# Performance work log

Measured on AMD Instinct MI355X. Metric: run time of the kernel, lower is better.

The kernel has to match this reference:

```python
import jax, jax.numpy as jnp
import numpy as np

EPS = 1e-5  # float32 path of the torch LayerNorm variants


def setup_inputs() -> dict:
    key = jax.random.key(0)
    ks = jax.random.split(key, 12)
    b, c, t, h, w = 2, 512, 16, 32, 32
    heads, dim_head = 8, 64
    inner = heads * dim_head            # 512
    cpb = c // 2                        # 256 (ContinuousPositionBias hidden dim)
    inner_ff = int(c * 4 * 2 / 3)       # 1365 (GEGLU FeedForward)
    s = 0.02
    return {
        "x": jax.random.normal(ks[0], (b, c, t, h, w), jnp.float32),
        "framerate": 4,
        "g_norm": jnp.ones((c,), jnp.float32),
        "Wq": jax.random.normal(ks[1], (c, inner), jnp.float32) * s,
        "Wkv": jax.random.normal(ks[2], (c, 2 * inner), jnp.float32) * s,
        "Wo": jax.random.normal(ks[3], (inner, c), jnp.float32) * s,
        "pos_emb": jax.random.normal(ks[4], (1, 30, c), jnp.float32),
        "fr_emb": jax.random.normal(ks[5], (1, 30, c), jnp.float32),
        "cpb_w1": jax.random.normal(ks[6], (1, cpb), jnp.float32) * s,
        "cpb_b1": jnp.zeros((cpb,), jnp.float32),
        "cpb_w2": jax.random.normal(ks[7], (cpb, cpb), jnp.float32) * s,
        "cpb_b2": jnp.zeros((cpb,), jnp.float32),
        "cpb_w3": jax.random.normal(ks[8], (cpb, 8), jnp.float32) * s,
        "cpb_b3": jnp.zeros((8,), jnp.float32),
        "Win": jax.random.normal(ks[9], (c, 2 * inner_ff), jnp.float32) * s,
        "chan_g": jnp.ones((inner_ff,), jnp.float32),
        "Wout": jax.random.normal(ks[10], (inner_ff, c), jnp.float32) * s,
    }


def _forward(x, framerate, g_norm, Wq, Wkv, Wo, pos_emb, fr_emb,
             cpb_w1, cpb_b1, cpb_w2, cpb_b2, cpb_w3, cpb_b3,
             Win, chan_g, Wout):
    b, c, t, hh, ww = x.shape
    heads = cpb_b3.shape[0]
    dim_head = Wq.shape[1] // heads
    scale = dim_head ** -0.5

    # ---- ContinuousPositionBias over time (num_dims=1, log_dist) ----
    pos = jnp.arange(t)
    rel = (pos[:, None] - pos[None, :])[..., None].astype(x.dtype)   # [t, t, 1]
    rel = jnp.sign(rel) * jnp.log(jnp.abs(rel) + 1.0)
    hb = jax.nn.silu(rel @ cpb_w1 + cpb_b1)
    hb = jax.nn.silu(hb @ cpb_w2 + cpb_b2)
    bias = jnp.transpose(hb @ cpb_w3 + cpb_b3, (2, 0, 1))            # [H, t, t]

    # ---- temporal attention: fold spatial dims into batch ----
    xt = jnp.transpose(x, (0, 3, 4, 2, 1)).reshape(b * hh * ww, t, c)  # [B, t, c]
    xe = xt + pos_emb[:, :t] + fr_emb[:, framerate - 1:framerate]
    # LayerNorm as written in the source: stats over dim=1 (the token axis)
    mean = jnp.mean(xe, axis=1, keepdims=True)
    var = jnp.var(xe, axis=1, keepdims=True)
    xn = (xe - mean) * jax.lax.rsqrt(jnp.maximum(var, EPS)) * g_norm

    q = (xn @ Wq).reshape(-1, t, heads, dim_head).transpose(0, 2, 1, 3)  # [B,H,t,d]
    k, v = jnp.split(xn @ Wkv, 2, axis=-1)
    k = k.reshape(-1, t, heads, dim_head).transpose(0, 2, 1, 3)
    v = v.reshape(-1, t, heads, dim_head).transpose(0, 2, 1, 3)

    sim = jnp.einsum('bhid,bhjd->bhij', q * scale, k) + bias[None]
    attn = jax.nn.softmax(sim, axis=-1)
    o = jnp.einsum('bhij,bhjd->bhid', attn, v)
    o = o.transpose(0, 2, 1, 3).reshape(-1, t, heads * dim_head) @ Wo
    xt = o + xt  # residual
    x = jnp.transpose(xt.reshape(b, hh, ww, t, c), (0, 4, 3, 1, 2))  # [b,c,t,h,w]

    # ---- GEGLU FeedForward (1x1x1 convs) with token shift over time ----
    y = jnp.einsum('bcthw,co->bothw', x, Win)
    y1, gate = jnp.split(y, 2, axis=1)
    y = y1 * jax.nn.gelu(gate, approximate=False)
    half = (y.shape[1] + 1) // 2  # torch.chunk: first chunk gets ceil
    ya, yb = y[:, :half], y[:, half:]
    yb = jnp.pad(yb, ((0, 0), (0, 0), (1, 0), (0, 0), (0, 0)))[:, :, :-1]
    y = jnp.concatenate([ya, yb], axis=1)
    m = jnp.mean(y, axis=1, keepdims=True)
    vv = jnp.var(y, axis=1, keepdims=True)
    y = (y - m) * jax.lax.rsqrt(jnp.maximum(vv, EPS)) * chan_g[None, :, None, None, None]
    y = jnp.einsum('bcthw,co->bothw', y, Wout)
    return y + x


def reference(x, framerate, g_norm, Wq, Wkv, Wo, pos_emb, fr_emb,
              cpb_w1, cpb_b1, cpb_w2, cpb_b2, cpb_w3, cpb_b3,
              Win, chan_g, Wout):
    return _forward(x, framerate, g_norm, Wq, Wkv, Wo, pos_emb, fr_emb,
                    cpb_w1, cpb_b1, cpb_w2, cpb_b2, cpb_w3, cpb_b3,
                    Win, chan_g, Wout)
```

## Files before the change

kernel.cpp:

```cpp
#include <hip/hip_runtime.h>

using u16 = unsigned short;
using f32x4 = __attribute__((ext_vector_type(4))) float;
using short8 = __attribute__((ext_vector_type(8))) short;

__device__ __forceinline__ float bf2f(u16 u) {
    union { unsigned int i; float f; } v; v.i = ((unsigned int)u) << 16; return v.f;
}
__device__ __forceinline__ u16 f2bf(float f) {
    union { float f; unsigned int i; } v; v.f = f;
    unsigned int u = v.i;
    u += 0x7fffu + ((u >> 16) & 1u);
    return (u16)(u >> 16);
}
__device__ __forceinline__ void gload16(const u16* g, u16* l) {
    __builtin_amdgcn_global_load_lds((const __attribute__((address_space(1))) void*)g,
                                     (__attribute__((address_space(3))) void*)l, 16, 0, 0);
}

__global__ __launch_bounds__(256) void prologue_all(
    const float* __restrict__ x, const int* __restrict__ frp,
    const float* __restrict__ g_norm, const float* __restrict__ pos_emb,
    const float* __restrict__ fr_emb,
    const float* __restrict__ Wq, const float* __restrict__ Wkv,
    const float* __restrict__ Wo, const float* __restrict__ Win,
    const float* __restrict__ Wout, const float* __restrict__ cg,
    const float* __restrict__ w1, const float* __restrict__ b1,
    const float* __restrict__ w2, const float* __restrict__ b2,
    const float* __restrict__ w3, const float* __restrict__ b3,
    u16* __restrict__ xn, u16* __restrict__ xt,
    u16* __restrict__ wqkvt, u16* __restrict__ wot,
    u16* __restrict__ winp, u16* __restrict__ woutt,
    float* __restrict__ ssum, float* __restrict__ bias)
{
    __shared__ __align__(16) char smem[256 * 36 * 2];
    const int bid = blockIdx.x;
    const int tid = threadIdx.x;
    if (bid < 2048) {
        u16* tile = (u16*)smem;
        const int b = bid >> 10, rem = bid & 1023;
        const int hw0 = (rem >> 4) << 4;
        const int c0 = (rem & 15) << 5;
        const int hwl = tid & 15, cl = tid >> 4;
        const int fr = frp[0] - 1;
        float v[2][16], mean2[2], ri2[2], gg2[2], fv2[2];
        for (int cp = 0; cp < 2; ++cp) {
            const int c = c0 + cl + (cp << 4);
            const float* xp = x + (size_t)(b * 512 + c) * 16384 + hw0 + hwl;
            const float fv = fr_emb[fr * 512 + c];
            float s1 = 0.f, s2 = 0.f;
#pragma unroll
            for (int t = 0; t < 16; ++t) {
                float xv = xp[t * 1024];
                v[cp][t] = xv;
                float xe = xv + pos_emb[t * 512 + c] + fv;
                s1 += xe; s2 += xe * xe;
            }
            float m = s1 * 0.0625f;
            float var = s2 * 0.0625f - m * m;
            mean2[cp] = m; ri2[cp] = rsqrtf(fmaxf(var, 1e-5f));
            gg2[cp] = g_norm[c]; fv2[cp] = fv;
        }
        for (int cp = 0; cp < 2; ++cp) {
            const int c = c0 + cl + (cp << 4);
#pragma unroll
            for (int t = 0; t < 16; ++t) {
                float xe = v[cp][t] + pos_emb[t * 512 + c] + fv2[cp];
                tile[((t << 4) + hwl) * 36 + cl + (cp << 4)] = f2bf((xe - mean2[cp]) * ri2[cp] * gg2[cp]);
            }
        }
        __syncthreads();
        for (int it = 0; it < 8; ++it) {
            int idx = it * 256 + tid;
            int rowl = idx >> 3, c4 = (idx & 7) << 2;
            size_t p = (size_t)b * 16384 + (size_t)(rowl >> 4) * 1024 + hw0 + (rowl & 15);
            uint2 d = *(const uint2*)(tile + rowl * 36 + c4);
            *(uint2*)(xn + p * 512 + c0 + c4) = d;
        }
        __syncthreads();
        for (int cp = 0; cp < 2; ++cp)
#pragma unroll
            for (int t = 0; t < 16; ++t)
                tile[((t << 4) + hwl) * 36 + cl + (cp << 4)] = f2bf(v[cp][t]);
        __syncthreads();
        for (int it = 0; it < 8; ++it) {
            int idx = it * 256 + tid;
            int rowl = idx >> 3, c4 = (idx & 7) << 2;
            size_t p = (size_t)b * 16384 + (size_t)(rowl >> 4) * 1024 + hw0 + (rowl & 15);
            uint2 d = *(const uint2*)(tile + rowl * 36 + c4);
            *(uint2*)(xt + p * 512 + c0 + c4) = d;
        }
        return;
    }
    if (bid < 2832) {
        float* tf = (float*)smem;
        const u16* dummy = nullptr; (void)dummy;
        int r0, c0, ldout;
        u16* dst;
        int kind;
        int tt;
        if (bid < 2240)      { tt = bid - 2048; r0 = (tt >> 3) << 6; c0 = (tt & 7) << 6;  dst = wqkvt; ldout = 512;  kind = 0; }
        else if (bid < 2304) { tt = bid - 2240; r0 = (tt >> 3) << 6; c0 = (tt & 7) << 6;  dst = wot;   ldout = 512;  kind = 1; }
        else if (bid < 2656) { tt = bid - 2304; r0 = (tt >> 3) << 6; c0 = (tt & 7) << 6;  dst = winp;  ldout = 512;  kind = 2; }
        else                 { tt = bid - 2656; r0 = (tt / 22) << 6; c0 = (tt % 22) << 6; dst = woutt; ldout = 1408; kind = 3; }
#pragma unroll 1
        for (int i = 0; i < 16; ++i) {
            int idx = tid + (i << 8);
            int cl = idx >> 6, rl = idx & 63;
            int r = r0 + rl, c = c0 + cl;
            float v;
            if (kind == 0) {
                v = (r < 512) ? Wq[c * 512 + r] : Wkv[c * 1024 + (r - 512)];
            } else if (kind == 1) {
                v = Wo[c * 512 + r];
            } else if (kind == 2) {
                int jj = ((r >> 5) << 4) + (r & 15);
                int gate = (r >> 4) & 1;
                v = (jj < 1365) ? Win[c * 2730 + jj + gate * 1365] : 0.f;
            } else {
                v = (c < 1365) ? Wout[c * 512 + r] * cg[c] : 0.f;
            }
            tf[rl * 65 + cl] = v;
        }
        __syncthreads();
        for (int i = 0; i < 4; ++i) {
            int idx = tid + (i << 8);
            int rl = idx >> 4, c4 = (idx & 15) << 2;
            const float* tp = tf + rl * 65 + c4;
            unsigned int lo = ((unsigned int)f2bf(tp[1]) << 16) | f2bf(tp[0]);
            unsigned int hi = ((unsigned int)f2bf(tp[3]) << 16) | f2bf(tp[2]);
            *(uint2*)(dst + (size_t)(r0 + rl) * ldout + c0 + c4) = make_uint2(lo, hi);
        }
        return;
    }
    if (bid < 2960) {
        int c = ((bid - 2832) << 2) + (tid >> 6);
        int lane = tid & 63;
        float s = 0.f;
        for (int j = lane; j < 1365; j += 64) s += Wout[j * 512 + c] * cg[j];
        for (int off = 32; off; off >>= 1) s += __shfl_xor(s, off);
        if (lane == 0) ssum[c] = s;
        return;
    }
    {
        float* h1 = (float*)smem;
        float* h2 = h1 + 256;
        int rc = bid - 2960;
        int ti = rc >> 4, tj = rc & 15;
        int j = tid;
        float r = (float)(ti - tj);
        float rl = (r > 0.f) ? logf(r + 1.f) : ((r < 0.f) ? -logf(1.f - r) : 0.f);
        float a = rl * w1[j] + b1[j];
        h1[j] = a / (1.f + __expf(-a));
        __syncthreads();
        float acc = b2[j];
        for (int k = 0; k < 256; ++k) acc += h1[k] * w2[k * 256 + j];
        h2[j] = acc / (1.f + __expf(-acc));
        __syncthreads();
        if (j < 8) {
            float ab = b3[j];
            for (int k = 0; k < 256; ++k) ab += h2[k] * w3[k * 8 + j];
            bias[j * 256 + ti * 16 + tj] = ab;
        }
    }
}

template<int EPI>
__global__ __launch_bounds__(256, 2) void gemm_bt(
    const u16* __restrict__ A, const u16* __restrict__ B, int K, int Nb,
    u16* __restrict__ outb, float* __restrict__ outf,
    const u16* __restrict__ addb,
    const float* __restrict__ ssum, int ldOut)
{
    __shared__ u16 lds[2 * 128 * 64];
    __shared__ float smr[256];
    u16* lA = lds;
    u16* lB = lds + 128 * 64;
    const int tid = threadIdx.x, lane = tid & 63, w = tid >> 6;
    const int wr = w >> 1, wc = w & 1;
    const int cpx = gridDim.x >> 3;
    const int wgid = (blockIdx.x & 7) * cpx + (blockIdx.x >> 3);
    const int p0 = (wgid / Nb) * 128, n0 = (wgid % Nb) * 128;
    f32x4 acc[4][4] = {};
    float sst[4] = {}, sq[4] = {};
    for (int kt = 0; kt < K; kt += 64) {
        for (int i = 0; i < 4; ++i) {
            int rb = w * 4 + i;
            int r = rb * 8 + (lane >> 3);
            int cg = (lane & 7) ^ (r & 7);
            gload16(A + (size_t)(p0 + r) * K + (kt + cg * 8), lA + rb * 512);
            gload16(B + (size_t)(n0 + r) * K + (kt + cg * 8), lB + rb * 512);
        }
        __syncthreads();
#pragma unroll
        for (int kk = 0; kk < 2; ++kk) {
            short8 av[4], bv[4];
#pragma unroll
            for (int m = 0; m < 4; ++m) {
                int r = wr * 64 + m * 16 + (lane & 15);
                int cc = ((kk << 2) + (lane >> 4)) ^ (r & 7);
                av[m] = *(const short8*)(lA + r * 64 + cc * 8);
            }
#pragma unroll
            for (int n = 0; n < 4; ++n) {
                int r = wc * 64 + n * 16 + (lane & 15);
                int cc = ((kk << 2) + (lane >> 4)) ^ (r & 7);
                bv[n] = *(const short8*)(lB + r * 64 + cc * 8);
            }
            if constexpr (EPI == 3) {
                if (wc == 0) {
#pragma unroll
                    for (int m = 0; m < 4; ++m)
#pragma unroll
                        for (int j = 0; j < 8; ++j) {
                            float v = bf2f((u16)av[m][j]);
                            sst[m] += v; sq[m] += v * v;
                        }
                }
            }
#pragma unroll
            for (int m = 0; m < 4; ++m)
#pragma unroll
                for (int n = 0; n < 4; ++n)
                    acc[m][n] = __builtin_amdgcn_mfma_f32_16x16x32_bf16(av[m], bv[n], acc[m][n], 0, 0, 0);
        }
        __syncthreads();
    }

    if constexpr (EPI == 0 || EPI == 1) {
#pragma unroll
        for (int m = 0; m < 4; ++m)
#pragma unroll
            for (int n = 0; n < 4; ++n) {
                int row = p0 + wr * 64 + m * 16 + ((lane >> 4) << 2);
                int col = n0 + wc * 64 + n * 16 + (lane & 15);
#pragma unroll
                for (int r = 0; r < 4; ++r) {
                    float vv = acc[m][n][r];
                    if constexpr (EPI == 1) vv += bf2f(addb[(size_t)(row + r) * ldOut + col]);
                    outb[(size_t)(row + r) * ldOut + col] = f2bf(vv);
                }
            }
    } else if constexpr (EPI == 2) {
#pragma unroll
        for (int m = 0; m < 4; ++m)
#pragma unroll
            for (int np = 0; np < 2; ++np) {
                int nv = np << 1;
                int colBase = n0 + wc * 64 + nv * 16 + (lane & 15);
                int jj = ((colBase >> 5) << 4) + (colBase & 15);
                int rowb = p0 + wr * 64 + m * 16 + ((lane >> 4) << 2);
                int t = (rowb >> 10) & 15;
#pragma unroll
                for (int r = 0; r < 4; ++r) {
                    int p = rowb + r;
                    float vv = acc[m][nv][r], gv = acc[m][nv + 1][r];
                    float glu = vv * 0.5f * gv * (1.f + erff(gv * 0.70710678f));
                    if (jj >= 1365) {
                        outb[(size_t)p * 1408 + jj] = 0;
                    } else if (jj >= 683) {
                        if (t < 15) outb[(size_t)(p + 1024) * 1408 + jj] = f2bf(glu);
                        if (t == 0) outb[(size_t)p * 1408 + jj] = 0;
                    } else {
                        outb[(size_t)p * 1408 + jj] = f2bf(glu);
                    }
                }
            }
    } else {
        if (wc == 0) {
#pragma unroll
            for (int m = 0; m < 4; ++m) {
                float s = sst[m], q = sq[m];
                s += __shfl_xor(s, 16); q += __shfl_xor(q, 16);
                s += __shfl_xor(s, 32); q += __shfl_xor(q, 32);
                if ((lane >> 4) == 0) {
                    int row = wr * 64 + m * 16 + (lane & 15);
                    smr[row] = s; smr[128 + row] = q;
                }
            }
        }
        __syncthreads();
        if (tid < 128) {
            float mm = smr[tid] * (1.f / 1365.f);
            float var = smr[128 + tid] * (1.f / 1365.f) - mm * mm;
            smr[tid] = mm;
            smr[128 + tid] = rsqrtf(fmaxf(var, 1e-5f));
        }
        float* ldsT = (float*)lds;
        const int bb = p0 >> 14, tt = (p0 >> 10) & 15, hwb = p0 & 1023;
        float* outp = outf + (size_t)bb * 8388608 + (size_t)tt * 1024 + hwb;
        for (int cg4 = 0; cg4 < 4; ++cg4) {
            __syncthreads();
            if (wc == (cg4 >> 1)) {
#pragma unroll
                for (int m = 0; m < 4; ++m)
#pragma unroll
                    for (int nn = 0; nn < 2; ++nn) {
                        int n = ((cg4 & 1) << 1) + nn;
                        int cl2 = (nn << 4) + (lane & 15);
                        int col = n0 + wc * 64 + n * 16 + (lane & 15);
                        int rl = wr * 64 + m * 16 + ((lane >> 4) << 2);
                        float ssv = ssum[col];
#pragma unroll
                        for (int r = 0; r < 4; ++r) {
                            int p = p0 + rl + r;
                            float vv = smr[128 + rl + r] * (acc[m][n][r] - smr[rl + r] * ssv)
                                     + bf2f(addb[(size_t)p * 512 + col]);
                            ldsT[cl2 * 132 + rl + r] = vv;
                        }
                    }
            }
            __syncthreads();
#pragma unroll
            for (int e = 0; e < 16; ++e) {
                int li = e * 256 + tid;
                int cl2 = li >> 7, hwl = li & 127;
                outp[(size_t)(n0 + cg4 * 32 + cl2) * 16384 + hwl] = ldsT[cl2 * 132 + hwl];
            }
        }
    }
}

__global__ __launch_bounds__(256, 2) void attn_kernel(
    const u16* __restrict__ qkv, const float* __restrict__ bias, u16* __restrict__ o)
{
    __shared__ u16 qkvt[3 * 128 * 64];
    __shared__ float pl[128 * 17];
    __shared__ float bl[256];
    const int tid = threadIdx.x, lane = tid & 63, w = tid >> 6;
    const int pc = blockIdx.x, h = blockIdx.y;
    const int b = pc >> 7, hw0 = (pc & 127) << 3;
    bl[tid] = bias[h * 256 + tid];
    for (int i = 0; i < 12; ++i) {
        int idx = w * 12 + i;
        int s = idx >> 4, rb = idx & 15;
        int r = (rb << 3) + (lane >> 3);
        int cg = (lane & 7) ^ (r & 7);
        size_t grow = (size_t)b * 16384 + (size_t)(r >> 3) * 1024 + hw0 + (r & 7);
        gload16(qkv + grow * 1536 + s * 512 + h * 64 + cg * 8, qkvt + s * 8192 + rb * 512);
    }
    __syncthreads();
    {
        const int qrow = tid & 127, hh = tid >> 7;
        const int pix = qrow & 7, ti = qrow >> 3;
        float qv[64];
        const u16* qr = qkvt + qrow * 64;
#pragma unroll
        for (int cc = 0; cc < 8; ++cc) {
            short8 qq = *(const short8*)(qr + ((cc ^ (qrow & 7)) << 3));
#pragma unroll
            for (int j = 0; j < 8; ++j) qv[cc * 8 + j] = bf2f((u16)qq[j]);
        }
#pragma unroll
        for (int tj8 = 0; tj8 < 8; ++tj8) {
            int tj = (hh << 3) + tj8;
            int rk = (tj << 3) + pix;
            const u16* kr = qkvt + 8192 + rk * 64;
            float a = 0.f;
#pragma unroll
            for (int cc = 0; cc < 8; ++cc) {
                short8 kk = *(const short8*)(kr + ((cc ^ (rk & 7)) << 3));
#pragma unroll
                for (int j = 0; j < 8; ++j) a += qv[cc * 8 + j] * bf2f((u16)kk[j]);
            }
            pl[qrow * 17 + tj] = a * 0.125f + bl[(ti << 4) + tj];
        }
    }
    __syncthreads();
    if (tid < 128) {
        float sc[16];
#pragma unroll
        for (int j = 0; j < 16; ++j) sc[j] = pl[tid * 17 + j];
        float mx = sc[0];
#pragma unroll
        for (int j = 1; j < 16; ++j) mx = fmaxf(mx, sc[j]);
        float sum = 0.f;
#pragma unroll
        for (int j = 0; j < 16; ++j) { sc[j] = __expf(sc[j] - mx); sum += sc[j]; }
        float inv = 1.f / sum;
#pragma unroll
        for (int j = 0; j < 16; ++j) pl[tid * 17 + j] = sc[j] * inv;
    }
    __syncthreads();
    {
        const int pix = tid >> 5, dg = tid & 31;
        float v0[16], v1[16];
#pragma unroll
        for (int tj = 0; tj < 16; ++tj) {
            int rv = (tj << 3) + pix;
            unsigned int d = *(const unsigned int*)(qkvt + 16384 + rv * 64 +
                               (((dg >> 2) ^ (rv & 7)) << 3) + ((dg & 3) << 1));
            v0[tj] = bf2f((u16)(d & 0xffff));
            v1[tj] = bf2f((u16)(d >> 16));
        }
#pragma unroll
        for (int ti = 0; ti < 16; ++ti) {
            float a0 = 0.f, a1 = 0.f;
            const float* pr = pl + ((ti << 3) + pix) * 17;
#pragma unroll
            for (int tj = 0; tj < 16; ++tj) {
                float pv = pr[tj];
                a0 += pv * v0[tj];
                a1 += pv * v1[tj];
            }
            size_t p = (size_t)b * 16384 + (size_t)ti * 1024 + hw0 + pix;
            unsigned int pk = (unsigned int)f2bf(a0) | ((unsigned int)f2bf(a1) << 16);
            *(unsigned int*)(o + p * 512 + h * 64 + (dg << 1)) = pk;
        }
    }
}

extern "C" void kernel_launch(void* const* d_in, const int* in_sizes, int n_in,
                              void* d_out, int out_size, void* d_ws, size_t ws_size,
                              hipStream_t stream)
{
    const float* x       = (const float*)d_in[0];
    const int*   frp     = (const int*)d_in[1];
    const float* g_norm  = (const float*)d_in[2];
    const float* Wq      = (const float*)d_in[3];
    const float* Wkv     = (const float*)d_in[4];
    const float* Wo      = (const float*)d_in[5];
    const float* pos_emb = (const float*)d_in[6];
    const float* fr_emb  = (const float*)d_in[7];
    const float* w1      = (const float*)d_in[8];
    const float* b1      = (const float*)d_in[9];
    const float* w2      = (const float*)d_in[10];
    const float* b2      = (const float*)d_in[11];
    const float* w3      = (const float*)d_in[12];
    const float* b3      = (const float*)d_in[13];
    const float* Win     = (const float*)d_in[14];
    const float* chan_g  = (const float*)d_in[15];
    const float* Wout    = (const float*)d_in[16];

    char* ws = (char*)d_ws;
    u16*   wqkvt = (u16*)(ws + 0);
    u16*   wot   = (u16*)(ws + 1572864);
    u16*   winp  = (u16*)(ws + 2097152);
    u16*   woutt = (u16*)(ws + 4980736);
    float* ssum  = (float*)(ws + 6422528);
    float* biasb = (float*)(ws + 6424576);
    u16*   qkv   = (u16*)(ws + 8388608);
    u16*   xn    = (u16*)(ws + 109051904);
    u16*   xt    = (u16*)(ws + 142606336);
    u16*   x2    = (u16*)(ws + 176160768);
    u16*   o_att = xn;
    u16*   yg    = qkv;

    prologue_all<<<3216, 256, 0, stream>>>(
        x, frp, g_norm, pos_emb, fr_emb,
        Wq, Wkv, Wo, Win, Wout, chan_g, w1, b1, w2, b2, w3, b3,
        xn, xt, wqkvt, wot, winp, woutt, ssum, biasb);
    gemm_bt<0><<<256 * 12, 256, 0, stream>>>(xn, wqkvt, 512, 12, qkv, nullptr, nullptr,
                                             nullptr, 1536);
    attn_kernel<<<dim3(256, 8), 256, 0, stream>>>(qkv, biasb, o_att);
    gemm_bt<1><<<256 * 4, 256, 0, stream>>>(o_att, wot, 512, 4, x2, nullptr, xt,
                                            nullptr, 512);
    gemm_bt<2><<<256 * 22, 256, 0, stream>>>(x2, winp, 512, 22, yg, nullptr, nullptr,
                                             nullptr, 1408);
    gemm_bt<3><<<256 * 4, 256, 0, stream>>>(yg, woutt, 1408, 4, nullptr, (float*)d_out, x2,
                                            ssum, 512);
}
```

Measured before the change: 402.2 us.

## Fuse QKV projection GEMM into temporal attention kernel per head tile

Reorders the packed QKV weight so each head's Q,K,V columns are contiguous, then computes the 128x192 QKV tile for one (pixel-group, head) inside the attention kernel and keeps it in LDS. This removes the separate QKV GEMM launch and the round trip of the large qkv intermediate through global memory. The cost is a bigger LDS footprint per block (about 58KB), which may lower occupancy, and a GEMM with a smaller N tile that reloads the A tile once per head.

```diff
diff --git a/kernel.cpp b/kernel.cpp
--- a/kernel.cpp
+++ b/kernel.cpp
@@ -94,7 +94,6 @@
     }
     if (bid < 2832) {
         float* tf = (float*)smem;
-        const u16* dummy = nullptr; (void)dummy;
         int r0, c0, ldout;
         u16* dst;
         int kind;
@@ -110,7 +109,11 @@
             int r = r0 + rl, c = c0 + cl;
             float v;
             if (kind == 0) {
-                v = (r < 512) ? Wq[c * 512 + r] : Wkv[c * 1024 + (r - 512)];
+                int h = r / 192, wch = r - h * 192;
+                int s = wch >> 6, d = wch & 63;
+                int oc = h * 64 + d;
+                v = (s == 0) ? Wq[c * 512 + oc]
+                             : Wkv[c * 1024 + (s - 1) * 512 + oc];
             } else if (kind == 1) {
                 v = Wo[c * 512 + r];
             } else if (kind == 2) {
@@ -161,6 +164,152 @@
             float ab = b3[j];
             for (int k = 0; k < 256; ++k) ab += h2[k] * w3[k * 8 + j];
             bias[j * 256 + ti * 16 + tj] = ab;
+        }
+    }
+}
+
+__global__ __launch_bounds__(256, 2) void gemm_qkv_attn(
+    const u16* __restrict__ A, const u16* __restrict__ B,
+    const float* __restrict__ bias, u16* __restrict__ o)
+{
+    __shared__ __align__(16) char smem[58880];
+    u16* lA = (u16*)smem;
+    u16* lB = (u16*)(smem + 16384);
+    u16* qkvt = (u16*)smem;
+    float* pl = (float*)(smem + 49152);
+    float* bl = (float*)(smem + 57856);
+    const int tid = threadIdx.x, lane = tid & 63, w = tid >> 6;
+    const int wr = w >> 1, wc = w & 1;
+    const int l15 = lane & 15, l16 = lane >> 4;
+    const int bidf = ((blockIdx.x & 7) << 8) + (blockIdx.x >> 3);
+    const int hwc = bidf >> 3, h = bidf & 7;
+    const int b = hwc >> 7, hw0 = (hwc & 127) << 3;
+    const u16* Bg = B + (size_t)h * 192 * 512;
+
+    bl[tid] = bias[h * 256 + tid];
+
+    f32x4 acc[4][6] = {};
+    for (int kt = 0; kt < 512; kt += 64) {
+        for (int i = 0; i < 4; ++i) {
+            int rb = w * 4 + i;
+            int r = rb * 8 + (lane >> 3);
+            int cg = (lane & 7) ^ (r & 7);
+            size_t p = (size_t)b * 16384 + (size_t)(r >> 3) * 1024 + hw0 + (r & 7);
+            gload16(A + p * 512 + kt + cg * 8, lA + rb * 512);
+        }
+        for (int i = 0; i < 6; ++i) {
+            int rb = w * 6 + i;
+            int r = rb * 8 + (lane >> 3);
+            int cg = (lane & 7) ^ (r & 7);
+            gload16(Bg + (size_t)r * 512 + kt + cg * 8, lB + rb * 512);
+        }
+        __syncthreads();
+#pragma unroll
+        for (int kk = 0; kk < 2; ++kk) {
+            short8 av[4], bv[6];
+#pragma unroll
+            for (int m = 0; m < 4; ++m) {
+                int r = wr * 64 + m * 16 + l15;
+                int cc = ((kk << 2) + l16) ^ (r & 7);
+                av[m] = *(const short8*)(lA + r * 64 + cc * 8);
+            }
+#pragma unroll
+            for (int n = 0; n < 6; ++n) {
+                int r = wc * 96 + n * 16 + l15;
+                int cc = ((kk << 2) + l16) ^ (r & 7);
+                bv[n] = *(const short8*)(lB + r * 64 + cc * 8);
+            }
+#pragma unroll
+            for (int m = 0; m < 4; ++m)
+#pragma unroll
+                for (int n = 0; n < 6; ++n)
+                    acc[m][n] = __builtin_amdgcn_mfma_f32_16x16x32_bf16(av[m], bv[n], acc[m][n], 0, 0, 0);
+        }
+        __syncthreads();
+    }
+
+#pragma unroll
+    for (int m = 0; m < 4; ++m)
+#pragma unroll
+        for (int n = 0; n < 6; ++n) {
+            int rl = wr * 64 + m * 16 + (l16 << 2);
+            int nc = wc * 96 + n * 16 + l15;
+            int s = nc >> 6, d = nc & 63;
+#pragma unroll
+            for (int r = 0; r < 4; ++r) {
+                int row = rl + r;
+                qkvt[s * 8192 + row * 64 + ((((d >> 3) ^ (row & 7))) << 3) + (d & 7)] =
+                    f2bf(acc[m][n][r]);
+            }
+        }
+    __syncthreads();
+
+    {
+        const int qrow = tid & 127, hh = tid >> 7;
+        const int pix = qrow & 7, ti = qrow >> 3;
+        float qv[64];
+        const u16* qr = qkvt + qrow * 64;
+#pragma unroll
+        for (int cc = 0; cc < 8; ++cc) {
+            short8 qq = *(const short8*)(qr + ((cc ^ (qrow & 7)) << 3));
+#pragma unroll
+            for (int j = 0; j < 8; ++j) qv[cc * 8 + j] = bf2f((u16)qq[j]);
+        }
+#pragma unroll
+        for (int tj8 = 0; tj8 < 8; ++tj8) {
+            int tj = (hh << 3) + tj8;
+            int rk = (tj << 3) + pix;
+            const u16* kr = qkvt + 8192 + rk * 64;
+            float a = 0.f;
+#pragma unroll
+            for (int cc = 0; cc < 8; ++cc) {
+                short8 kk = *(const short8*)(kr + ((cc ^ (rk & 7)) << 3));
+#pragma unroll
+                for (int j = 0; j < 8; ++j) a += qv[cc * 8 + j] * bf2f((u16)kk[j]);
+            }
+            pl[qrow * 17 + tj] = a * 0.125f + bl[(ti << 4) + tj];
+        }
+    }
+    __syncthreads();
+    if (tid < 128) {
+        float sc[16];
+#pragma unroll
+        for (int j = 0; j < 16; ++j) sc[j] = pl[tid * 17 + j];
+        float mx = sc[0];
+#pragma unroll
+        for (int j = 1; j < 16; ++j) mx = fmaxf(mx, sc[j]);
+        float sum = 0.f;
+#pragma unroll
+        for (int j = 0; j < 16; ++j) { sc[j] = __expf(sc[j] - mx); sum += sc[j]; }
+        float inv = 1.f / sum;
+#pragma unroll
+        for (int j = 0; j < 16; ++j) pl[tid * 17 + j] = sc[j] * inv;
+    }
+    __syncthreads();
+    {
+        const int pix = tid >> 5, dg = tid & 31;
+        float v0[16], v1[16];
+#pragma unroll
+        for (int tj = 0; tj < 16; ++tj) {
+            int rv = (tj << 3) + pix;
+            unsigned int d = *(const unsigned int*)(qkvt + 16384 + rv * 64 +
+                               (((dg >> 2) ^ (rv & 7)) << 3) + ((dg & 3) << 1));
+            v0[tj] = bf2f((u16)(d & 0xffff));
+            v1[tj] = bf2f((u16)(d >> 16));
+        }
+#pragma unroll
+        for (int ti = 0; ti < 16; ++ti) {
+            float a0 = 0.f, a1 = 0.f;
+            const float* pr = pl + ((ti << 3) + pix) * 17;
+#pragma unroll
+            for (int tj = 0; tj < 16; ++tj) {
+                float pv = pr[tj];
+                a0 += pv * v0[tj];
+                a1 += pv * v1[tj];
+            }
+            size_t p = (size_t)b * 16384 + (size_t)ti * 1024 + hw0 + pix;
+            unsigned int pk = (unsigned int)f2bf(a0) | ((unsigned int)f2bf(a1) << 16);
+            *(unsigned int*)(o + p * 512 + h * 64 + (dg << 1)) = pk;
         }
     }
 }
@@ -227,7 +376,7 @@
         __syncthreads();
     }
 
-    if constexpr (EPI == 0 || EPI == 1) {
+    if constexpr (EPI == 1) {
 #pragma unroll
         for (int m = 0; m < 4; ++m)
 #pragma unroll
@@ -236,8 +385,7 @@
                 int col = n0 + wc * 64 + n * 16 + (lane & 15);
 #pragma unroll
                 for (int r = 0; r < 4; ++r) {
-                    float vv = acc[m][n][r];
-                    if constexpr (EPI == 1) vv += bf2f(addb[(size_t)(row + r) * ldOut + col]);
+                    float vv = acc[m][n][r] + bf2f(addb[(size_t)(row + r) * ldOut + col]);
                     outb[(size_t)(row + r) * ldOut + col] = f2bf(vv);
                 }
             }
@@ -317,95 +465,6 @@
                 int cl2 = li >> 7, hwl = li & 127;
                 outp[(size_t)(n0 + cg4 * 32 + cl2) * 16384 + hwl] = ldsT[cl2 * 132 + hwl];
             }
-        }
-    }
-}
-
-__global__ __launch_bounds__(256, 2) void attn_kernel(
-    const u16* __restrict__ qkv, const float* __restrict__ bias, u16* __restrict__ o)
-{
-    __shared__ u16 qkvt[3 * 128 * 64];
-    __shared__ float pl[128 * 17];
-    __shared__ float bl[256];
-    const int tid = threadIdx.x, lane = tid & 63, w = tid >> 6;
-    const int pc = blockIdx.x, h = blockIdx.y;
-    const int b = pc >> 7, hw0 = (pc & 127) << 3;
-    bl[tid] = bias[h * 256 + tid];
-    for (int i = 0; i < 12; ++i) {
-        int idx = w * 12 + i;
-        int s = idx >> 4, rb = idx & 15;
-        int r = (rb << 3) + (lane >> 3);
-        int cg = (lane & 7) ^ (r & 7);
-        size_t grow = (size_t)b * 16384 + (size_t)(r >> 3) * 1024 + hw0 + (r & 7);
-        gload16(qkv + grow * 1536 + s * 512 + h * 64 + cg * 8, qkvt + s * 8192 + rb * 512);
-    }
-    __syncthreads();
-    {
-        const int qrow = tid & 127, hh = tid >> 7;
-        const int pix = qrow & 7, ti = qrow >> 3;
-        float qv[64];
-        const u16* qr = qkvt + qrow * 64;
-#pragma unroll
-        for (int cc = 0; cc < 8; ++cc) {
-            short8 qq = *(const short8*)(qr + ((cc ^ (qrow & 7)) << 3));
-#pragma unroll
-            for (int j = 0; j < 8; ++j) qv[cc * 8 + j] = bf2f((u16)qq[j]);
-        }
-#pragma unroll
-        for (int tj8 = 0; tj8 < 8; ++tj8) {
-            int tj = (hh << 3) + tj8;
-            int rk = (tj << 3) + pix;
-            const u16* kr = qkvt + 8192 + rk * 64;
-            float a = 0.f;
-#pragma unroll
-            for (int cc = 0; cc < 8; ++cc) {
-                short8 kk = *(const short8*)(kr + ((cc ^ (rk & 7)) << 3));
-#pragma unroll
-                for (int j = 0; j < 8; ++j) a += qv[cc * 8 + j] * bf2f((u16)kk[j]);
-            }
-            pl[qrow * 17 + tj] = a * 0.125f + bl[(ti << 4) + tj];
-        }
-    }
-    __syncthreads();
-    if (tid < 128) {
-        float sc[16];
-#pragma unroll
-        for (int j = 0; j < 16; ++j) sc[j] = pl[tid * 17 + j];
-        float mx = sc[0];
-#pragma unroll
-        for (int j = 1; j < 16; ++j) mx = fmaxf(mx, sc[j]);
-        float sum = 0.f;
-#pragma unroll
-        for (int j = 0; j < 16; ++j) { sc[j] = __expf(sc[j] - mx); sum += sc[j]; }
-        float inv = 1.f / sum;
-#pragma unroll
-        for (int j = 0; j < 16; ++j) pl[tid * 17 + j] = sc[j] * inv;
-    }
-    __syncthreads();
-    {
-        const int pix = tid >> 5, dg = tid & 31;
-        float v0[16], v1[16];
-#pragma unroll
-        for (int tj = 0; tj < 16; ++tj) {
-            int rv = (tj << 3) + pix;
-            unsigned int d = *(const unsigned int*)(qkvt + 16384 + rv * 64 +
-                               (((dg >> 2) ^ (rv & 7)) << 3) + ((dg & 3) << 1));
-            v0[tj] = bf2f((u16)(d & 0xffff));
-            v1[tj] = bf2f((u16)(d >> 16));
-        }
-#pragma unroll
-        for (int ti = 0; ti < 16; ++ti) {
-            float a0 = 0.f, a1 = 0.f;
-            const float* pr = pl + ((ti << 3) + pix) * 17;
-#pragma unroll
-            for (int tj = 0; tj < 16; ++tj) {
-                float pv = pr[tj];
-                a0 += pv * v0[tj];
-                a1 += pv * v1[tj];
-            }
-            size_t p = (size_t)b * 16384 + (size_t)ti * 1024 + hw0 + pix;
-            unsigned int pk = (unsigned int)f2bf(a0) | ((unsigned int)f2bf(a1) << 16);
-            *(unsigned int*)(o + p * 512 + h * 64 + (dg << 1)) = pk;
         }
     }
 }
@@ -439,20 +498,18 @@
     u16*   woutt = (u16*)(ws + 4980736);
     float* ssum  = (float*)(ws + 6422528);
     float* biasb = (float*)(ws + 6424576);
-    u16*   qkv   = (u16*)(ws + 8388608);
+    u16*   big   = (u16*)(ws + 8388608);
     u16*   xn    = (u16*)(ws + 109051904);
     u16*   xt    = (u16*)(ws + 142606336);
     u16*   x2    = (u16*)(ws + 176160768);
-    u16*   o_att = xn;
-    u16*   yg    = qkv;
+    u16*   o_att = big;
+    u16*   yg    = big;
 
     prologue_all<<<3216, 256, 0, stream>>>(
         x, frp, g_norm, pos_emb, fr_emb,
         Wq, Wkv, Wo, Win, Wout, chan_g, w1, b1, w2, b2, w3, b3,
         xn, xt, wqkvt, wot, winp, woutt, ssum, biasb);
-    gemm_bt<0><<<256 * 12, 256, 0, stream>>>(xn, wqkvt, 512, 12, qkv, nullptr, nullptr,
-                                             nullptr, 1536);
-    attn_kernel<<<dim3(256, 8), 256, 0, stream>>>(qkv, biasb, o_att);
+    gemm_qkv_attn<<<2048, 256, 0, stream>>>(xn, wqkvt, biasb, o_att);
     gemm_bt<1><<<256 * 4, 256, 0, stream>>>(o_att, wot, 512, 4, x2, nullptr, xt,
                                             nullptr, 512);
     gemm_bt<2><<<256 * 22, 256, 0, stream>>>(x2, winp, 512, 22, yg, nullptr, nullptr,
```

Result: faster. 391.3 us, median of 2 (-2.7%).
